# Kernel tuning notes

Hardware: AMD Instinct MI355X
Metric: run time of the kernel (lower is better)

Reference implementation:

```python
import jax, jax.numpy as jnp
import numpy as np

B, C, NA = 32, 9, 65440
GAMMA = 3.0
SCALE_XY = 1.0 / 0.1
SCALE_WH = 1.0 / 0.2


def setup_inputs() -> dict:
    key = jax.random.key(0)
    k1, k2, k3, k4, k5 = jax.random.split(key, 5)
    bbox_delta = jax.random.normal(k1, (B, 4, NA), dtype=jnp.float32)
    confs = jax.random.normal(k2, (B, C, NA), dtype=jnp.float32)
    # gt boxes in xywh, keep w/h strictly positive for the log() in _loc_vec
    gt_bbox = jax.random.uniform(k3, (B, NA, 4), dtype=jnp.float32, minval=0.05, maxval=1.0)
    gt_labels = jax.random.randint(k4, (B, NA), 0, C, dtype=jnp.int32)
    anchors = jax.random.uniform(k5, (1, 4, NA), dtype=jnp.float32, minval=0.1, maxval=1.0)
    return {"bbox_delta": bbox_delta, "confs": confs, "gt_bbox": gt_bbox,
            "gt_labels": gt_labels, "anchors": anchors}


def reference(bbox_delta, confs, gt_bbox, gt_labels, anchors):
    n_classes = confs.shape[1]
    # ---- focal classification loss (fused: no one-hot materialized) ----
    # alpha = [10, 1000, ..., 1000]; einsum 'a,bcd->bad' followed by sum(dim=1)
    # collapses to multiplying by sum(alpha) since y is one-hot over c.
    alpha = jnp.full((n_classes,), 1000.0, dtype=jnp.float32).at[0].set(10.0)
    logp = jax.nn.log_softmax(confs, axis=1)              # [B,C,N]
    t = gt_labels.astype(jnp.int32)[:, None, :]           # [B,1,N]
    logp_t = jnp.take_along_axis(logp, t, axis=1)[:, 0, :]  # [B,N]
    p_t = jnp.exp(logp_t)
    focal = (1.0 - p_t) ** GAMMA * logp_t                 # [B,N]
    classification_loss = jnp.mean(-jnp.sum(alpha) * focal)

    # ---- localization loss (masked smooth-L1, no boolean compaction) ----
    gt_t = jnp.transpose(gt_bbox, (0, 2, 1))               # [B,4,N]
    gxy = SCALE_XY * (gt_t[:, :2, :] - anchors[:, :2, :]) / anchors[:, 2:, :]
    gwh = SCALE_WH * jnp.log(gt_t[:, 2:, :] / anchors[:, 2:, :])
    gt_loc = jnp.concatenate([gxy, gwh], axis=1)           # [B,4,N]

    pos = gt_labels > 0                                    # [B,N]
    mask = pos[:, None, :]                                 # broadcast over 4 coords
    diff = jnp.where(mask, bbox_delta - gt_loc, 0.0)
    ad = jnp.abs(diff)
    sl1 = jnp.where(ad < 1.0, 0.5 * diff * diff, ad - 0.5)
    regression_loss = jnp.sum(jnp.where(mask, sl1, 0.0))
    num_pos = jnp.sum(pos).astype(jnp.float32)

    total_loss = regression_loss / num_pos + classification_loss
    return total_loss
```

## Files before the change

kernel.cpp:

```cpp
#include <hip/hip_runtime.h>
#include <math.h>

constexpr int B  = 32;
constexpr int C  = 9;
constexpr int NA = 65440;
constexpr int PER_B    = NA / 4;
constexpr int NTHREADS = B * PER_B;
constexpr int BLOCK    = 256;
constexpr int GRID     = NTHREADS / BLOCK;

constexpr int WS_REG = 2048;
constexpr int WS_POS = 4096;

__device__ __forceinline__ float4 ld4(const float* p) {
    return *reinterpret_cast<const float4*>(p);
}

__device__ __forceinline__ float smooth_l1(float d) {
    float ad = fabsf(d);
    return ad < 1.0f ? 0.5f * d * d : ad - 0.5f;
}

typedef __attribute__((address_space(3))) void       lds_void_t;
typedef const __attribute__((address_space(1))) void gbl_void_t;

__global__ __launch_bounds__(BLOCK, 4) void ssd_main(
    const float* __restrict__ bbox_delta,
    const float* __restrict__ confs,
    const float* __restrict__ gt_bbox,
    const int*   __restrict__ gt_labels,
    const float* __restrict__ anchors,
    float* __restrict__ ws)
{
    __shared__ float conf_lds[C][BLOCK * 4];

    const int tid = blockIdx.x * BLOCK + threadIdx.x;
    const int b   = tid / PER_B;
    const int a   = (tid - b * PER_B) * 4;
    const int wid = threadIdx.x >> 6;

    const int4 lab = *reinterpret_cast<const int4*>(gt_labels + (size_t)b * NA + a);

    const float* abase = anchors + a;
    float4 ax = ld4(abase);
    float4 ay = ld4(abase + NA);
    float4 aw = ld4(abase + 2 * NA);
    float4 ah = ld4(abase + 3 * NA);

    const float* dbase = bbox_delta + (size_t)b * 4 * NA + a;
    float4 d0 = ld4(dbase);
    float4 d1 = ld4(dbase + NA);
    float4 d2 = ld4(dbase + 2 * NA);
    float4 d3 = ld4(dbase + 3 * NA);

    const float* gbase = gt_bbox + ((size_t)b * NA + a) * 4;
    float4 g0 = ld4(gbase);
    float4 g1 = ld4(gbase + 4);
    float4 g2 = ld4(gbase + 8);
    float4 g3 = ld4(gbase + 12);

    __builtin_amdgcn_sched_barrier(0);

    const float* cg = confs + (size_t)b * C * NA + a;
#pragma unroll
    for (int c = 0; c < C; ++c) {
        __builtin_amdgcn_global_load_lds(
            (gbl_void_t*)(cg + (size_t)c * NA),
            (lds_void_t*)(&conf_lds[c][wid * 256]),
            16, 0, 0);
    }
    __builtin_amdgcn_sched_barrier(0);

    float reg = 0.f, pcnt = 0.f;
#define DO_ANCHOR(GT, AXC, AYC, AWC, AHC, D0C, D1C, D2C, D3C, LABC)               \
    {                                                                             \
        float gx = 10.0f * __fdividef(GT.x - AXC, AWC);                           \
        float gy = 10.0f * __fdividef(GT.y - AYC, AHC);                           \
        float gw = 5.0f * __logf(__fdividef(GT.z, AWC));                          \
        float gh = 5.0f * __logf(__fdividef(GT.w, AHC));                          \
        float s  = smooth_l1(D0C - gx) + smooth_l1(D1C - gy) +                    \
                   smooth_l1(D2C - gw) + smooth_l1(D3C - gh);                     \
        if (LABC > 0) { reg += s; pcnt += 1.0f; }                                 \
    }
    DO_ANCHOR(g0, ax.x, ay.x, aw.x, ah.x, d0.x, d1.x, d2.x, d3.x, lab.x)
    DO_ANCHOR(g1, ax.y, ay.y, aw.y, ah.y, d0.y, d1.y, d2.y, d3.y, lab.y)
    DO_ANCHOR(g2, ax.z, ay.z, aw.z, ah.z, d0.z, d1.z, d2.z, d3.z, lab.z)
    DO_ANCHOR(g3, ax.w, ay.w, aw.w, ah.w, d0.w, d1.w, d2.w, d3.w, lab.w)
#undef DO_ANCHOR

    asm volatile("s_waitcnt vmcnt(0)" ::: "memory");
    __builtin_amdgcn_sched_barrier(0);

    float4 cf[C];
#pragma unroll
    for (int c = 0; c < C; ++c)
        cf[c] = *reinterpret_cast<const float4*>(&conf_lds[c][threadIdx.x * 4]);

    float sex = 0.f, sey = 0.f, sez = 0.f, sew = 0.f;
    float ctx = cf[0].x, cty = cf[0].y, ctz = cf[0].z, ctw = cf[0].w;
#pragma unroll
    for (int c = 0; c < C; ++c) {
        sex += __expf(cf[c].x);
        sey += __expf(cf[c].y);
        sez += __expf(cf[c].z);
        sew += __expf(cf[c].w);
        ctx = (lab.x == c) ? cf[c].x : ctx;
        cty = (lab.y == c) ? cf[c].y : cty;
        ctz = (lab.z == c) ? cf[c].z : ctz;
        ctw = (lab.w == c) ? cf[c].w : ctw;
    }
    float lpx = ctx - __logf(sex);
    float lpy = cty - __logf(sey);
    float lpz = ctz - __logf(sez);
    float lpw = ctw - __logf(sew);

    float focal;
    {
        float px = __expf(lpx), py = __expf(lpy), pz = __expf(lpz), pw = __expf(lpw);
        float ox = 1.f - px, oy = 1.f - py, oz = 1.f - pz, ow = 1.f - pw;
        focal = ox*ox*ox*lpx + oy*oy*oy*lpy + oz*oz*oz*lpz + ow*ow*ow*lpw;
    }

#pragma unroll
    for (int off = 32; off > 0; off >>= 1) {
        focal += __shfl_down(focal, off, 64);
        reg   += __shfl_down(reg,   off, 64);
        pcnt  += __shfl_down(pcnt,  off, 64);
    }
    __shared__ float sf[4], sr[4], sp[4];
    const int lane = threadIdx.x & 63;
    if (lane == 0) { sf[wid] = focal; sr[wid] = reg; sp[wid] = pcnt; }
    __syncthreads();
    if (threadIdx.x == 0) {
        ws[blockIdx.x]          = sf[0] + sf[1] + sf[2] + sf[3];
        ws[WS_REG + blockIdx.x] = sr[0] + sr[1] + sr[2] + sr[3];
        ws[WS_POS + blockIdx.x] = sp[0] + sp[1] + sp[2] + sp[3];
    }
}

__global__ __launch_bounds__(256) void finalize_k(const float* __restrict__ ws,
                                                  float* __restrict__ out) {
    float F = 0.f, R = 0.f, P = 0.f;
    for (int i = threadIdx.x; i < GRID; i += 256) {
        F += ws[i];
        R += ws[WS_REG + i];
        P += ws[WS_POS + i];
    }
#pragma unroll
    for (int off = 32; off > 0; off >>= 1) {
        F += __shfl_down(F, off, 64);
        R += __shfl_down(R, off, 64);
        P += __shfl_down(P, off, 64);
    }
    __shared__ float sf[4], sr[4], sp[4];
    const int wid  = threadIdx.x >> 6;
    const int lane = threadIdx.x & 63;
    if (lane == 0) { sf[wid] = F; sr[wid] = R; sp[wid] = P; }
    __syncthreads();
    if (threadIdx.x == 0) {
        float Ft = sf[0] + sf[1] + sf[2] + sf[3];
        float Rt = sr[0] + sr[1] + sr[2] + sr[3];
        float Pt = sp[0] + sp[1] + sp[2] + sp[3];
        const float inv_n = 1.0f / (float)((size_t)B * NA);
        out[0] = Rt / Pt - 8010.0f * Ft * inv_n;
    }
}

extern "C" void kernel_launch(void* const* d_in, const int* in_sizes, int n_in,
                              void* d_out, int out_size, void* d_ws, size_t ws_size,
                              hipStream_t stream) {
    const float* bbox_delta = (const float*)d_in[0];
    const float* confs      = (const float*)d_in[1];
    const float* gt_bbox    = (const float*)d_in[2];
    const int*   gt_labels  = (const int*)d_in[3];
    const float* anchors    = (const float*)d_in[4];
    float* ws  = (float*)d_ws;
    float* out = (float*)d_out;

    ssd_main<<<GRID, BLOCK, 0, stream>>>(bbox_delta, confs, gt_bbox, gt_labels, anchors, ws);
    finalize_k<<<1, 256, 0, stream>>>(ws, out);
}
```

Before: 172.6 us.

## Stage all inputs through LDS with direct global loads in single-wave blocks

Every input stream (labels, anchors, deltas, gt boxes and confidences) is now loaded with global_load_lds into a per-block LDS staging buffer. Before, only the confidences took that path and the rest went through vector register loads. Blocks shrink to a single 64-thread wave, so the cross-wave shared-memory reduction and __syncthreads are gone and each block writes its partial sums straight to the workspace. The workspace offsets grow to fit the larger grid. The aim is to get all loads in flight at once and drop barrier cost, but each wave now needs more LDS, which may cap how many waves fit on a CU.

Measured after the change: 179.2 us. +3.8%, slower.

```diff
diff --git a/kernel.cpp b/kernel.cpp
--- a/kernel.cpp
+++ b/kernel.cpp
@@ -6,15 +6,11 @@
 constexpr int NA = 65440;
 constexpr int PER_B    = NA / 4;
 constexpr int NTHREADS = B * PER_B;
-constexpr int BLOCK    = 256;
+constexpr int BLOCK    = 64;
 constexpr int GRID     = NTHREADS / BLOCK;
 
-constexpr int WS_REG = 2048;
-constexpr int WS_POS = 4096;
-
-__device__ __forceinline__ float4 ld4(const float* p) {
-    return *reinterpret_cast<const float4*>(p);
-}
+constexpr int WS_REG = 8192;
+constexpr int WS_POS = 16384;
 
 __device__ __forceinline__ float smooth_l1(float d) {
     float ad = fabsf(d);
@@ -24,7 +20,7 @@
 typedef __attribute__((address_space(3))) void       lds_void_t;
 typedef const __attribute__((address_space(1))) void gbl_void_t;
 
-__global__ __launch_bounds__(BLOCK, 4) void ssd_main(
+__global__ __launch_bounds__(BLOCK) void ssd_main(
     const float* __restrict__ bbox_delta,
     const float* __restrict__ confs,
     const float* __restrict__ gt_bbox,
@@ -32,44 +28,77 @@
     const float* __restrict__ anchors,
     float* __restrict__ ws)
 {
-    __shared__ float conf_lds[C][BLOCK * 4];
+    __shared__ float4 stage[22][BLOCK];
 
-    const int tid = blockIdx.x * BLOCK + threadIdx.x;
-    const int b   = tid / PER_B;
-    const int a   = (tid - b * PER_B) * 4;
-    const int wid = threadIdx.x >> 6;
-
-    const int4 lab = *reinterpret_cast<const int4*>(gt_labels + (size_t)b * NA + a);
-
-    const float* abase = anchors + a;
-    float4 ax = ld4(abase);
-    float4 ay = ld4(abase + NA);
-    float4 aw = ld4(abase + 2 * NA);
-    float4 ah = ld4(abase + 3 * NA);
-
-    const float* dbase = bbox_delta + (size_t)b * 4 * NA + a;
-    float4 d0 = ld4(dbase);
-    float4 d1 = ld4(dbase + NA);
-    float4 d2 = ld4(dbase + 2 * NA);
-    float4 d3 = ld4(dbase + 3 * NA);
-
-    const float* gbase = gt_bbox + ((size_t)b * NA + a) * 4;
-    float4 g0 = ld4(gbase);
-    float4 g1 = ld4(gbase + 4);
-    float4 g2 = ld4(gbase + 8);
-    float4 g3 = ld4(gbase + 12);
-
-    __builtin_amdgcn_sched_barrier(0);
+    const int lane = threadIdx.x;
+    const int tid  = blockIdx.x * BLOCK + lane;
+    const int b    = tid / PER_B;
+    const int a    = (tid - b * PER_B) * 4;
 
     const float* cg = confs + (size_t)b * C * NA + a;
 #pragma unroll
+    for (int c = 0; c < C; ++c)
+        __builtin_amdgcn_global_load_lds((gbl_void_t*)(cg + (size_t)c * NA),
+                                         (lds_void_t*)&stage[c][0], 16, 0, 0);
+
+    __builtin_amdgcn_global_load_lds((gbl_void_t*)(gt_labels + (size_t)b * NA + a),
+                                     (lds_void_t*)&stage[9][0], 16, 0, 0);
+
+    const float* ab = anchors + a;
+#pragma unroll
+    for (int r = 0; r < 4; ++r)
+        __builtin_amdgcn_global_load_lds((gbl_void_t*)(ab + (size_t)r * NA),
+                                         (lds_void_t*)&stage[10 + r][0], 16, 0, 0);
+
+    const float* db = bbox_delta + (size_t)b * 4 * NA + a;
+#pragma unroll
+    for (int r = 0; r < 4; ++r)
+        __builtin_amdgcn_global_load_lds((gbl_void_t*)(db + (size_t)r * NA),
+                                         (lds_void_t*)&stage[14 + r][0], 16, 0, 0);
+
+    const float* gb = gt_bbox + ((size_t)b * NA + a) * 4;
+#pragma unroll
+    for (int j = 0; j < 4; ++j)
+        __builtin_amdgcn_global_load_lds((gbl_void_t*)(gb + 4 * j),
+                                         (lds_void_t*)&stage[18 + j][0], 16, 0, 0);
+
+    asm volatile("s_waitcnt vmcnt(0)" ::: "memory");
+    __builtin_amdgcn_sched_barrier(0);
+
+    const int4 lab = reinterpret_cast<const int4*>(&stage[9][0])[lane];
+
+    float sex = 0.f, sey = 0.f, sez = 0.f, sew = 0.f;
+    float ctx = 0.f, cty = 0.f, ctz = 0.f, ctw = 0.f;
+#pragma unroll
     for (int c = 0; c < C; ++c) {
-        __builtin_amdgcn_global_load_lds(
-            (gbl_void_t*)(cg + (size_t)c * NA),
-            (lds_void_t*)(&conf_lds[c][wid * 256]),
-            16, 0, 0);
+        float4 cf = stage[c][lane];
+        sex += __expf(cf.x);
+        sey += __expf(cf.y);
+        sez += __expf(cf.z);
+        sew += __expf(cf.w);
+        ctx = (lab.x == c) ? cf.x : ctx;
+        cty = (lab.y == c) ? cf.y : cty;
+        ctz = (lab.z == c) ? cf.z : ctz;
+        ctw = (lab.w == c) ? cf.w : ctw;
     }
-    __builtin_amdgcn_sched_barrier(0);
+    float lpx = ctx - __logf(sex);
+    float lpy = cty - __logf(sey);
+    float lpz = ctz - __logf(sez);
+    float lpw = ctw - __logf(sew);
+
+    float focal;
+    {
+        float px = __expf(lpx), py = __expf(lpy), pz = __expf(lpz), pw = __expf(lpw);
+        float ox = 1.f - px, oy = 1.f - py, oz = 1.f - pz, ow = 1.f - pw;
+        focal = ox*ox*ox*lpx + oy*oy*oy*lpy + oz*oz*oz*lpz + ow*ow*ow*lpw;
+    }
+
+    const float4 ax = stage[10][lane], ay = stage[11][lane];
+    const float4 aw = stage[12][lane], ah = stage[13][lane];
+    const float4 d0 = stage[14][lane], d1 = stage[15][lane];
+    const float4 d2 = stage[16][lane], d3 = stage[17][lane];
+    const float4 g0 = stage[18][lane], g1 = stage[19][lane];
+    const float4 g2 = stage[20][lane], g3 = stage[21][lane];
 
     float reg = 0.f, pcnt = 0.f;
 #define DO_ANCHOR(GT, AXC, AYC, AWC, AHC, D0C, D1C, D2C, D3C, LABC)               \
@@ -88,53 +117,16 @@
     DO_ANCHOR(g3, ax.w, ay.w, aw.w, ah.w, d0.w, d1.w, d2.w, d3.w, lab.w)
 #undef DO_ANCHOR
 
-    asm volatile("s_waitcnt vmcnt(0)" ::: "memory");
-    __builtin_amdgcn_sched_barrier(0);
-
-    float4 cf[C];
-#pragma unroll
-    for (int c = 0; c < C; ++c)
-        cf[c] = *reinterpret_cast<const float4*>(&conf_lds[c][threadIdx.x * 4]);
-
-    float sex = 0.f, sey = 0.f, sez = 0.f, sew = 0.f;
-    float ctx = cf[0].x, cty = cf[0].y, ctz = cf[0].z, ctw = cf[0].w;
-#pragma unroll
-    for (int c = 0; c < C; ++c) {
-        sex += __expf(cf[c].x);
-        sey += __expf(cf[c].y);
-        sez += __expf(cf[c].z);
-        sew += __expf(cf[c].w);
-        ctx = (lab.x == c) ? cf[c].x : ctx;
-        cty = (lab.y == c) ? cf[c].y : cty;
-        ctz = (lab.z == c) ? cf[c].z : ctz;
-        ctw = (lab.w == c) ? cf[c].w : ctw;
-    }
-    float lpx = ctx - __logf(sex);
-    float lpy = cty - __logf(sey);
-    float lpz = ctz - __logf(sez);
-    float lpw = ctw - __logf(sew);
-
-    float focal;
-    {
-        float px = __expf(lpx), py = __expf(lpy), pz = __expf(lpz), pw = __expf(lpw);
-        float ox = 1.f - px, oy = 1.f - py, oz = 1.f - pz, ow = 1.f - pw;
-        focal = ox*ox*ox*lpx + oy*oy*oy*lpy + oz*oz*oz*lpz + ow*ow*ow*lpw;
-    }
-
 #pragma unroll
     for (int off = 32; off > 0; off >>= 1) {
         focal += __shfl_down(focal, off, 64);
         reg   += __shfl_down(reg,   off, 64);
         pcnt  += __shfl_down(pcnt,  off, 64);
     }
-    __shared__ float sf[4], sr[4], sp[4];
-    const int lane = threadIdx.x & 63;
-    if (lane == 0) { sf[wid] = focal; sr[wid] = reg; sp[wid] = pcnt; }
-    __syncthreads();
-    if (threadIdx.x == 0) {
-        ws[blockIdx.x]          = sf[0] + sf[1] + sf[2] + sf[3];
-        ws[WS_REG + blockIdx.x] = sr[0] + sr[1] + sr[2] + sr[3];
-        ws[WS_POS + blockIdx.x] = sp[0] + sp[1] + sp[2] + sp[3];
+    if (lane == 0) {
+        ws[blockIdx.x]          = focal;
+        ws[WS_REG + blockIdx.x] = reg;
+        ws[WS_POS + blockIdx.x] = pcnt;
     }
 }
 
```
